# Optimization experiments

Hardware: AMD Instinct MI355X
Metric: run time of the kernel (lower is better)

Reference implementation:

```python
import jax, jax.numpy as jnp
import numpy as np

B, C, W, H = 4, 256, 64, 64
AC = C // 4  # attn channels


def setup_inputs() -> dict:
    key = jax.random.key(0)
    ks = jax.random.split(key, 4)
    x = jax.random.normal(ks[0], (B, C, W, H), dtype=jnp.float32)
    Wq = jax.random.normal(ks[1], (AC, C), dtype=jnp.float32) * (1.0 / np.sqrt(C))
    Wk = jax.random.normal(ks[2], (AC, C), dtype=jnp.float32) * (1.0 / np.sqrt(C))
    Wv = jax.random.normal(ks[3], (C, C), dtype=jnp.float32) * (1.0 / np.sqrt(C))
    bq = jnp.zeros((AC,), dtype=jnp.float32)
    bk = jnp.zeros((AC,), dtype=jnp.float32)
    bv = jnp.zeros((C,), dtype=jnp.float32)
    gamma = jnp.zeros((1,), dtype=jnp.float32)
    return {"x": x, "Wq": Wq, "bq": bq, "Wk": Wk, "bk": bk, "Wv": Wv, "bv": bv, "gamma": gamma}


def reference(x, Wq, bq, Wk, bk, Wv, bv, gamma):
    b, c, w, h = x.shape
    n = w * h
    xf = x.reshape(b, c, n)  # [B, C, N]
    # 1x1 convs == channel GEMMs
    q = jnp.einsum('oc,bcn->bon', Wq, xf) + bq[None, :, None]  # [B, AC, N]
    k = jnp.einsum('oc,bcn->bon', Wk, xf) + bk[None, :, None]  # [B, AC, N]
    v = jnp.einsum('oc,bcn->bon', Wv, xf) + bv[None, :, None]  # [B, C, N]
    # attn[b, i, j] = sum_c q[b, c, i] * k[b, c, j]  (query transposed)
    attn = jnp.einsum('bci,bcj->bij', q, k)  # [B, N, N]
    # NOTE: non-standard softmax over dim=1 (over query index i for each column j)
    attn = jax.nn.softmax(attn, axis=1)
    # attn_out = attn @ value.T  -> [B, N, C]
    attn_out = jnp.einsum('bij,bcj->bic', attn, v)
    attn_out = attn_out.reshape(b, w, h, c).transpose(0, 3, 1, 2)  # [B, C, W, H]
    return gamma[0] * attn_out + x
```

## Files before the change

### kernel.cpp

```cpp
#include <hip/hip_runtime.h>
#include <hip/hip_bf16.h>

#define BB 4
#define CC 256
#define NN 4096
#define AC2 64

typedef __attribute__((ext_vector_type(4))) float f32x4;
typedef __attribute__((ext_vector_type(8))) short bf16x8;

__device__ __forceinline__ short f2bf(float f) {
    unsigned u = __builtin_bit_cast(unsigned, f);
    u = u + 0x7FFFu + ((u >> 16) & 1u);
    return (short)(u >> 16);
}

__global__ __launch_bounds__(256) void qkv_kernel(
    const float* __restrict__ x,
    const float* __restrict__ Wq, const float* __restrict__ bq,
    const float* __restrict__ Wk, const float* __restrict__ bk,
    const float* __restrict__ Wv, const float* __restrict__ bv,
    short* __restrict__ Qt, short* __restrict__ Kt, short* __restrict__ V)
{
    __shared__ __align__(16) short Wl[384 * 72];
    __shared__ __align__(16) short Xl[64 * 72];
    const int bid = blockIdx.x;
    const int b = bid >> 6;
    const int n0 = (bid & 63) << 6;
    const int tid = threadIdx.x;
    const int lane = tid & 63, w = tid >> 6;

    f32x4 acc[6][4];
#pragma unroll
    for (int i = 0; i < 6; ++i)
#pragma unroll
        for (int j = 0; j < 4; ++j) acc[i][j] = (f32x4){0.f, 0.f, 0.f, 0.f};

    for (int ck = 0; ck < 4; ++ck) {
        const int c0 = ck * 64;
#pragma unroll 4
        for (int t = 0; t < 16; ++t) {
            int idx = tid + t * 256;
            int cr = idx >> 6, nc = idx & 63;
            float v = x[(((size_t)b * CC + c0 + cr) * NN) + n0 + nc];
            Xl[nc * 72 + cr] = f2bf(v);
        }
#pragma unroll 8
        for (int t = 0; t < 96; ++t) {
            int idx = tid + t * 256;
            int o = idx >> 6, cc2 = idx & 63;
            const float* row = (o < 64) ? (Wq + o * CC)
                             : (o < 128) ? (Wk + (o - 64) * CC)
                                         : (Wv + (o - 128) * CC);
            Wl[o * 72 + cc2] = f2bf(row[c0 + cc2]);
        }
        __syncthreads();
#pragma unroll
        for (int ks = 0; ks < 2; ++ks) {
            const int co = ks * 32 + ((lane >> 4) << 3);
            bf16x8 Bf[4];
#pragma unroll
            for (int nf = 0; nf < 4; ++nf)
                Bf[nf] = *(const bf16x8*)&Xl[(nf * 16 + (lane & 15)) * 72 + co];
#pragma unroll
            for (int of = 0; of < 6; ++of) {
                bf16x8 Af = *(const bf16x8*)&Wl[((w * 6 + of) * 16 + (lane & 15)) * 72 + co];
#pragma unroll
                for (int nf = 0; nf < 4; ++nf)
                    acc[of][nf] = __builtin_amdgcn_mfma_f32_16x16x32_bf16(
                        Af, Bf[nf], acc[of][nf], 0, 0, 0);
            }
        }
        __syncthreads();
    }
#pragma unroll
    for (int of = 0; of < 6; ++of) {
        const int obase = (w * 6 + of) * 16 + ((lane >> 4) << 2);
        float bias[4];
#pragma unroll
        for (int r = 0; r < 4; ++r) {
            int o = obase + r;
            bias[r] = (o < 64) ? bq[o] : (o < 128) ? bk[o - 64] : bv[o - 128];
        }
#pragma unroll
        for (int nf = 0; nf < 4; ++nf) {
            const int n = n0 + nf * 16 + (lane & 15);
            if (obase < 128) {
                short4 pk;
                pk.x = f2bf(acc[of][nf][0] + bias[0]);
                pk.y = f2bf(acc[of][nf][1] + bias[1]);
                pk.z = f2bf(acc[of][nf][2] + bias[2]);
                pk.w = f2bf(acc[of][nf][3] + bias[3]);
                short* dst = (obase < 64)
                    ? (Qt + ((size_t)b * NN + n) * AC2 + obase)
                    : (Kt + ((size_t)b * NN + n) * AC2 + (obase - 64));
                *(short4*)dst = pk;
            } else {
#pragma unroll
                for (int r = 0; r < 4; ++r) {
                    int o = obase + r - 128;
                    V[(((size_t)b * CC + o) * NN) + n] = f2bf(acc[of][nf][r] + bias[r]);
                }
            }
        }
    }
}

__global__ __launch_bounds__(256) void stats_kernel(
    const short* __restrict__ Qt, const short* __restrict__ Kt,
    float* __restrict__ mArr, float* __restrict__ rlArr)
{
    const int bid = blockIdx.x;
    const int b = bid >> 8;
    const int j0 = (bid & 255) << 4;
    const int tid = threadIdx.x;
    const int lane = tid & 63, w = tid >> 6;

    bf16x8 Bf[2];
#pragma unroll
    for (int ks = 0; ks < 2; ++ks)
        Bf[ks] = *(const bf16x8*)&Kt[((size_t)b * NN + j0 + (lane & 15)) * AC2 +
                                     ks * 32 + ((lane >> 4) << 3)];

    float m_run = -INFINITY, l_run = 0.f;
    for (int ii = 0; ii < 16; ++ii) {
        const int i0 = w * 1024 + ii * 64;
        f32x4 s[4];
#pragma unroll
        for (int f = 0; f < 4; ++f) {
            const size_t rowA = (size_t)b * NN + i0 + f * 16 + (lane & 15);
            bf16x8 A0 = *(const bf16x8*)&Qt[rowA * AC2 + ((lane >> 4) << 3)];
            bf16x8 A1 = *(const bf16x8*)&Qt[rowA * AC2 + 32 + ((lane >> 4) << 3)];
            f32x4 t = (f32x4){0.f, 0.f, 0.f, 0.f};
            t = __builtin_amdgcn_mfma_f32_16x16x32_bf16(A0, Bf[0], t, 0, 0, 0);
            t = __builtin_amdgcn_mfma_f32_16x16x32_bf16(A1, Bf[1], t, 0, 0, 0);
            s[f] = t;
        }
        float mx = s[0][0];
#pragma unroll
        for (int f = 0; f < 4; ++f)
#pragma unroll
            for (int r = 0; r < 4; ++r) mx = fmaxf(mx, s[f][r]);
        const float m_new = fmaxf(m_run, mx);
        float add = 0.f;
#pragma unroll
        for (int f = 0; f < 4; ++f)
#pragma unroll
            for (int r = 0; r < 4; ++r) add += __expf(s[f][r] - m_new);
        l_run = l_run * __expf(m_run - m_new) + add;
        m_run = m_new;
    }
#pragma unroll
    for (int off = 16; off <= 32; off <<= 1) {
        float m2 = __shfl_xor(m_run, off);
        float l2 = __shfl_xor(l_run, off);
        float mm = fmaxf(m_run, m2);
        l_run = l_run * __expf(m_run - mm) + l2 * __expf(m2 - mm);
        m_run = mm;
    }
    __shared__ float sm[4][16];
    __shared__ float sl[4][16];
    if (lane < 16) { sm[w][lane] = m_run; sl[w][lane] = l_run; }
    __syncthreads();
    if (tid < 16) {
        float m = sm[0][tid], l = sl[0][tid];
#pragma unroll
        for (int q = 1; q < 4; ++q) {
            float m2 = sm[q][tid], l2 = sl[q][tid];
            float mm = fmaxf(m, m2);
            l = l * __expf(m - mm) + l2 * __expf(m2 - mm);
            m = mm;
        }
        mArr[(size_t)b * NN + j0 + tid] = m;
        rlArr[(size_t)b * NN + j0 + tid] = 1.f / l;
    }
}

__global__ __launch_bounds__(256) void out_kernel(
    const short* __restrict__ Qt, const short* __restrict__ Kt,
    const short* __restrict__ V,
    const float* __restrict__ mArr, const float* __restrict__ rlArr,
    const float* __restrict__ x, const float* __restrict__ gamma,
    float* __restrict__ out)
{
    __shared__ __align__(16) short Pl[64 * 72];
    const int bid = blockIdx.x;
    const int b = bid >> 6;
    const int i0 = (bid & 63) << 6;
    const int tid = threadIdx.x;
    const int lane = tid & 63, w = tid >> 6;

    bf16x8 Aq[2];
#pragma unroll
    for (int ks = 0; ks < 2; ++ks)
        Aq[ks] = *(const bf16x8*)&Qt[((size_t)b * NN + i0 + w * 16 + (lane & 15)) * AC2 +
                                     ks * 32 + ((lane >> 4) << 3)];

    f32x4 acc[4][4];
#pragma unroll
    for (int i = 0; i < 4; ++i)
#pragma unroll
        for (int j = 0; j < 4; ++j) acc[i][j] = (f32x4){0.f, 0.f, 0.f, 0.f};

    for (int jt = 0; jt < 64; ++jt) {
        const int j0 = jt * 64;
#pragma unroll
        for (int jf = 0; jf < 4; ++jf) {
            const int j = j0 + jf * 16 + (lane & 15);
            f32x4 s = (f32x4){0.f, 0.f, 0.f, 0.f};
#pragma unroll
            for (int ks = 0; ks < 2; ++ks) {
                bf16x8 Bf = *(const bf16x8*)&Kt[((size_t)b * NN + j) * AC2 +
                                                ks * 32 + ((lane >> 4) << 3)];
                s = __builtin_amdgcn_mfma_f32_16x16x32_bf16(Aq[ks], Bf, s, 0, 0, 0);
            }
            const float mj = mArr[(size_t)b * NN + j];
            const float rj = rlArr[(size_t)b * NN + j];
#pragma unroll
            for (int r = 0; r < 4; ++r) {
                float p = __expf(s[r] - mj) * rj;
                Pl[(w * 16 + ((lane >> 4) << 2) + r) * 72 + jf * 16 + (lane & 15)] = f2bf(p);
            }
        }
        __syncthreads();
#pragma unroll
        for (int ks = 0; ks < 2; ++ks) {
            const int jj = j0 + ks * 32 + ((lane >> 4) << 3);
            bf16x8 Bv[4];
#pragma unroll
            for (int cf = 0; cf < 4; ++cf) {
                const int c = w * 64 + cf * 16 + (lane & 15);
                Bv[cf] = *(const bf16x8*)&V[(((size_t)b * CC + c) * NN) + jj];
            }
#pragma unroll
            for (int f = 0; f < 4; ++f) {
                bf16x8 Ap = *(const bf16x8*)&Pl[(f * 16 + (lane & 15)) * 72 +
                                                ks * 32 + ((lane >> 4) << 3)];
#pragma unroll
                for (int cf = 0; cf < 4; ++cf)
                    acc[f][cf] = __builtin_amdgcn_mfma_f32_16x16x32_bf16(
                        Ap, Bv[cf], acc[f][cf], 0, 0, 0);
            }
        }
        __syncthreads();
    }
    const float g = gamma[0];
#pragma unroll
    for (int f = 0; f < 4; ++f) {
#pragma unroll
        for (int cf = 0; cf < 4; ++cf) {
            const int c = w * 64 + cf * 16 + (lane & 15);
#pragma unroll
            for (int r = 0; r < 4; ++r) {
                const int i = i0 + f * 16 + ((lane >> 4) << 2) + r;
                const size_t idx = ((size_t)b * CC + c) * NN + i;
                out[idx] = g * acc[f][cf][r] + x[idx];
            }
        }
    }
}

extern "C" void kernel_launch(void* const* d_in, const int* in_sizes, int n_in,
                              void* d_out, int out_size, void* d_ws, size_t ws_size,
                              hipStream_t stream) {
    const float* x     = (const float*)d_in[0];
    const float* Wq    = (const float*)d_in[1];
    const float* bq    = (const float*)d_in[2];
    const float* Wk    = (const float*)d_in[3];
    const float* bk    = (const float*)d_in[4];
    const float* Wv    = (const float*)d_in[5];
    const float* bv    = (const float*)d_in[6];
    const float* gamma = (const float*)d_in[7];
    float* out = (float*)d_out;

    short* Qt = (short*)d_ws;
    short* Kt = Qt + (size_t)BB * NN * AC2;
    short* V  = Kt + (size_t)BB * NN * AC2;
    float* mArr  = (float*)(V + (size_t)BB * CC * NN);
    float* rlArr = mArr + (size_t)BB * NN;

    qkv_kernel<<<BB * 64, 256, 0, stream>>>(x, Wq, bq, Wk, bk, Wv, bv, Qt, Kt, V);
    stats_kernel<<<BB * 256, 256, 0, stream>>>(Qt, Kt, mArr, rlArr);
    out_kernel<<<BB * 64, 256, 0, stream>>>(Qt, Kt, V, mArr, rlArr, x, gamma, out);
}
```

Before: 359.6 us.

## Split attention output across channel slices and pre-convert weights to bf16

Adds a prep kernel that converts the weights to bf16 once, so the QKV kernel loads weight fragments directly instead of staging them in shared memory, and uses 512-thread blocks over 32-column tiles. The output kernel now splits channels into four slices per query tile, giving four times as many blocks. Each wave keeps its own P tile, which removes the block barriers, and output is written as coalesced float4 through a shared-memory transpose. Softmax stats are folded into a single log-sum-exp value, and block ids are XCD-swizzled. The cost is that QK^T and exp are recomputed four times, once per channel slice.

```diff
diff --git a/kernel.cpp b/kernel.cpp
--- a/kernel.cpp
+++ b/kernel.cpp
@@ -15,67 +15,79 @@
     return (short)(u >> 16);
 }
 
-__global__ __launch_bounds__(256) void qkv_kernel(
-    const float* __restrict__ x,
-    const float* __restrict__ Wq, const float* __restrict__ bq,
-    const float* __restrict__ Wk, const float* __restrict__ bk,
-    const float* __restrict__ Wv, const float* __restrict__ bv,
+__global__ __launch_bounds__(256) void prep_kernel(
+    const float* __restrict__ Wq, const float* __restrict__ Wk,
+    const float* __restrict__ Wv, short* __restrict__ Wb)
+{
+    const int idx = (blockIdx.x * 256 + threadIdx.x) * 4;
+    const int o = idx >> 8, c = idx & 255;
+    const float* row = (o < 64) ? (Wq + o * CC)
+                     : (o < 128) ? (Wk + (o - 64) * CC)
+                                 : (Wv + (o - 128) * CC);
+    float4 v = *(const float4*)&row[c];
+    short4 s4;
+    s4.x = f2bf(v.x); s4.y = f2bf(v.y); s4.z = f2bf(v.z); s4.w = f2bf(v.w);
+    *(short4*)&Wb[idx] = s4;
+}
+
+__global__ __launch_bounds__(512) void qkv_kernel(
+    const float* __restrict__ x, const short* __restrict__ Wb,
+    const float* __restrict__ bq, const float* __restrict__ bk,
+    const float* __restrict__ bv,
     short* __restrict__ Qt, short* __restrict__ Kt, short* __restrict__ V)
 {
-    __shared__ __align__(16) short Wl[384 * 72];
-    __shared__ __align__(16) short Xl[64 * 72];
-    const int bid = blockIdx.x;
-    const int b = bid >> 6;
-    const int n0 = (bid & 63) << 6;
+    __shared__ __align__(16) short Xl[32 * 72];
+    const int bid0 = blockIdx.x;
+    const int bid = ((bid0 & 7) << 6) | (bid0 >> 3);
+    const int b = bid >> 7;
+    const int n0 = (bid & 127) << 5;
     const int tid = threadIdx.x;
     const int lane = tid & 63, w = tid >> 6;
-
-    f32x4 acc[6][4];
-#pragma unroll
-    for (int i = 0; i < 6; ++i)
-#pragma unroll
-        for (int j = 0; j < 4; ++j) acc[i][j] = (f32x4){0.f, 0.f, 0.f, 0.f};
+    const int l15 = lane & 15, lh = lane >> 4;
+
+    f32x4 acc[3][2];
+#pragma unroll
+    for (int i = 0; i < 3; ++i)
+#pragma unroll
+        for (int j = 0; j < 2; ++j) acc[i][j] = (f32x4){0.f, 0.f, 0.f, 0.f};
 
     for (int ck = 0; ck < 4; ++ck) {
-        const int c0 = ck * 64;
-#pragma unroll 4
-        for (int t = 0; t < 16; ++t) {
-            int idx = tid + t * 256;
-            int cr = idx >> 6, nc = idx & 63;
-            float v = x[(((size_t)b * CC + c0 + cr) * NN) + n0 + nc];
-            Xl[nc * 72 + cr] = f2bf(v);
-        }
-#pragma unroll 8
-        for (int t = 0; t < 96; ++t) {
-            int idx = tid + t * 256;
-            int o = idx >> 6, cc2 = idx & 63;
-            const float* row = (o < 64) ? (Wq + o * CC)
-                             : (o < 128) ? (Wk + (o - 64) * CC)
-                                         : (Wv + (o - 128) * CC);
-            Wl[o * 72 + cc2] = f2bf(row[c0 + cc2]);
+        const int c0 = ck << 6;
+        bf16x8 Af[3][2];
+#pragma unroll
+        for (int of = 0; of < 3; ++of)
+#pragma unroll
+            for (int ks = 0; ks < 2; ++ks)
+                Af[of][ks] = *(const bf16x8*)&Wb[(size_t)(w * 48 + of * 16 + l15) * CC +
+                                                 c0 + ks * 32 + (lh << 3)];
+        {
+            const int cr = tid >> 3, q4 = tid & 7;
+            float4 v = *(const float4*)&x[((size_t)(b * CC + c0 + cr)) * NN + n0 + q4 * 4];
+            Xl[(q4 * 4 + 0) * 72 + cr] = f2bf(v.x);
+            Xl[(q4 * 4 + 1) * 72 + cr] = f2bf(v.y);
+            Xl[(q4 * 4 + 2) * 72 + cr] = f2bf(v.z);
+            Xl[(q4 * 4 + 3) * 72 + cr] = f2bf(v.w);
         }
         __syncthreads();
 #pragma unroll
         for (int ks = 0; ks < 2; ++ks) {
-            const int co = ks * 32 + ((lane >> 4) << 3);
-            bf16x8 Bf[4];
-#pragma unroll
-            for (int nf = 0; nf < 4; ++nf)
-                Bf[nf] = *(const bf16x8*)&Xl[(nf * 16 + (lane & 15)) * 72 + co];
-#pragma unroll
-            for (int of = 0; of < 6; ++of) {
-                bf16x8 Af = *(const bf16x8*)&Wl[((w * 6 + of) * 16 + (lane & 15)) * 72 + co];
-#pragma unroll
-                for (int nf = 0; nf < 4; ++nf)
+            const int co = ks * 32 + (lh << 3);
+            bf16x8 Bf[2];
+#pragma unroll
+            for (int nf = 0; nf < 2; ++nf)
+                Bf[nf] = *(const bf16x8*)&Xl[(nf * 16 + l15) * 72 + co];
+#pragma unroll
+            for (int of = 0; of < 3; ++of)
+#pragma unroll
+                for (int nf = 0; nf < 2; ++nf)
                     acc[of][nf] = __builtin_amdgcn_mfma_f32_16x16x32_bf16(
-                        Af, Bf[nf], acc[of][nf], 0, 0, 0);
-            }
+                        Af[of][ks], Bf[nf], acc[of][nf], 0, 0, 0);
         }
         __syncthreads();
     }
 #pragma unroll
-    for (int of = 0; of < 6; ++of) {
-        const int obase = (w * 6 + of) * 16 + ((lane >> 4) << 2);
+    for (int of = 0; of < 3; ++of) {
+        const int obase = w * 48 + of * 16 + (lh << 2);
         float bias[4];
 #pragma unroll
         for (int r = 0; r < 4; ++r) {
@@ -83,8 +95,8 @@
             bias[r] = (o < 64) ? bq[o] : (o < 128) ? bk[o - 64] : bv[o - 128];
         }
 #pragma unroll
-        for (int nf = 0; nf < 4; ++nf) {
-            const int n = n0 + nf * 16 + (lane & 15);
+        for (int nf = 0; nf < 2; ++nf) {
+            const int n = n0 + nf * 16 + l15;
             if (obase < 128) {
                 short4 pk;
                 pk.x = f2bf(acc[of][nf][0] + bias[0]);
@@ -108,9 +120,10 @@
 
 __global__ __launch_bounds__(256) void stats_kernel(
     const short* __restrict__ Qt, const short* __restrict__ Kt,
-    float* __restrict__ mArr, float* __restrict__ rlArr)
+    float* __restrict__ tArr)
 {
-    const int bid = blockIdx.x;
+    const int bid0 = blockIdx.x;
+    const int bid = ((bid0 & 7) << 7) | (bid0 >> 3);
     const int b = bid >> 8;
     const int j0 = (bid & 255) << 4;
     const int tid = threadIdx.x;
@@ -171,92 +184,94 @@
             l = l * __expf(m - mm) + l2 * __expf(m2 - mm);
             m = mm;
         }
-        mArr[(size_t)b * NN + j0 + tid] = m;
-        rlArr[(size_t)b * NN + j0 + tid] = 1.f / l;
+        tArr[(size_t)b * NN + j0 + tid] = m + __logf(l);
     }
 }
 
 __global__ __launch_bounds__(256) void out_kernel(
     const short* __restrict__ Qt, const short* __restrict__ Kt,
     const short* __restrict__ V,
-    const float* __restrict__ mArr, const float* __restrict__ rlArr,
+    const float* __restrict__ tArr,
     const float* __restrict__ x, const float* __restrict__ gamma,
     float* __restrict__ out)
 {
-    __shared__ __align__(16) short Pl[64 * 72];
-    const int bid = blockIdx.x;
-    const int b = bid >> 6;
-    const int i0 = (bid & 63) << 6;
+    __shared__ __align__(16) short Pl[4 * 16 * 72];
+    __shared__ __align__(16) float Pf[4 * 16 * 69];
+    const int bid0 = blockIdx.x;
+    const int bid = ((bid0 & 7) << 7) | (bid0 >> 3);
+    const int cs = bid & 3;
+    const int itile = (bid >> 2) & 63;
+    const int b = bid >> 8;
+    const int i0 = itile << 6, c0 = cs << 6;
     const int tid = threadIdx.x;
     const int lane = tid & 63, w = tid >> 6;
+    const int l15 = lane & 15, lh = lane >> 4;
+    const int iw = i0 + (w << 4);
+    short* Plw = Pl + w * (16 * 72);
+
+    const short* Ktb = Kt + (size_t)b * NN * AC2;
+    const float* tb = tArr + (size_t)b * NN;
+    const short* Vb = V + ((size_t)b * CC + c0) * NN;
 
     bf16x8 Aq[2];
 #pragma unroll
     for (int ks = 0; ks < 2; ++ks)
-        Aq[ks] = *(const bf16x8*)&Qt[((size_t)b * NN + i0 + w * 16 + (lane & 15)) * AC2 +
-                                     ks * 32 + ((lane >> 4) << 3)];
-
-    f32x4 acc[4][4];
-#pragma unroll
-    for (int i = 0; i < 4; ++i)
-#pragma unroll
-        for (int j = 0; j < 4; ++j) acc[i][j] = (f32x4){0.f, 0.f, 0.f, 0.f};
+        Aq[ks] = *(const bf16x8*)&Qt[((size_t)b * NN + iw + l15) * AC2 +
+                                     ks * 32 + (lh << 3)];
+
+    f32x4 acc[4];
+#pragma unroll
+    for (int i = 0; i < 4; ++i) acc[i] = (f32x4){0.f, 0.f, 0.f, 0.f};
 
     for (int jt = 0; jt < 64; ++jt) {
         const int j0 = jt * 64;
 #pragma unroll
         for (int jf = 0; jf < 4; ++jf) {
-            const int j = j0 + jf * 16 + (lane & 15);
+            const int j = j0 + jf * 16 + l15;
             f32x4 s = (f32x4){0.f, 0.f, 0.f, 0.f};
 #pragma unroll
             for (int ks = 0; ks < 2; ++ks) {
-                bf16x8 Bf = *(const bf16x8*)&Kt[((size_t)b * NN + j) * AC2 +
-                                                ks * 32 + ((lane >> 4) << 3)];
+                bf16x8 Bf = *(const bf16x8*)&Ktb[(size_t)j * AC2 + ks * 32 + (lh << 3)];
                 s = __builtin_amdgcn_mfma_f32_16x16x32_bf16(Aq[ks], Bf, s, 0, 0, 0);
             }
-            const float mj = mArr[(size_t)b * NN + j];
-            const float rj = rlArr[(size_t)b * NN + j];
-#pragma unroll
-            for (int r = 0; r < 4; ++r) {
-                float p = __expf(s[r] - mj) * rj;
-                Pl[(w * 16 + ((lane >> 4) << 2) + r) * 72 + jf * 16 + (lane & 15)] = f2bf(p);
+            const float tj = tb[j];
+#pragma unroll
+            for (int r = 0; r < 4; ++r)
+                Plw[(lh * 4 + r) * 72 + jf * 16 + l15] = f2bf(__expf(s[r] - tj));
+        }
+#pragma unroll
+        for (int ks = 0; ks < 2; ++ks) {
+            const int jj = j0 + ks * 32 + (lh << 3);
+            bf16x8 Ap = *(const bf16x8*)&Plw[l15 * 72 + ks * 32 + (lh << 3)];
+#pragma unroll
+            for (int cf = 0; cf < 4; ++cf) {
+                bf16x8 Bv = *(const bf16x8*)&Vb[(size_t)(cf * 16 + l15) * NN + jj];
+                acc[cf] = __builtin_amdgcn_mfma_f32_16x16x32_bf16(Ap, Bv, acc[cf], 0, 0, 0);
             }
         }
-        __syncthreads();
-#pragma unroll
-        for (int ks = 0; ks < 2; ++ks) {
-            const int jj = j0 + ks * 32 + ((lane >> 4) << 3);
-            bf16x8 Bv[4];
-#pragma unroll
-            for (int cf = 0; cf < 4; ++cf) {
-                const int c = w * 64 + cf * 16 + (lane & 15);
-                Bv[cf] = *(const bf16x8*)&V[(((size_t)b * CC + c) * NN) + jj];
-            }
-#pragma unroll
-            for (int f = 0; f < 4; ++f) {
-                bf16x8 Ap = *(const bf16x8*)&Pl[(f * 16 + (lane & 15)) * 72 +
-                                                ks * 32 + ((lane >> 4) << 3)];
-#pragma unroll
-                for (int cf = 0; cf < 4; ++cf)
-                    acc[f][cf] = __builtin_amdgcn_mfma_f32_16x16x32_bf16(
-                        Ap, Bv[cf], acc[f][cf], 0, 0, 0);
-            }
-        }
-        __syncthreads();
-    }
+    }
+    float* Pfw = Pf + w * (16 * 69);
+#pragma unroll
+    for (int cf = 0; cf < 4; ++cf)
+#pragma unroll
+        for (int r = 0; r < 4; ++r)
+            Pfw[(lh * 4 + r) * 69 + cf * 16 + l15] = acc[cf][r];
     const float g = gamma[0];
-#pragma unroll
-    for (int f = 0; f < 4; ++f) {
-#pragma unroll
-        for (int cf = 0; cf < 4; ++cf) {
-            const int c = w * 64 + cf * 16 + (lane & 15);
-#pragma unroll
-            for (int r = 0; r < 4; ++r) {
-                const int i = i0 + f * 16 + ((lane >> 4) << 2) + r;
-                const size_t idx = ((size_t)b * CC + c) * NN + i;
-                out[idx] = g * acc[f][cf][r] + x[idx];
-            }
-        }
+    const size_t obase = ((size_t)(b * CC + c0 + lane)) * NN + iw;
+#pragma unroll
+    for (int e4 = 0; e4 < 4; ++e4) {
+        float4 v;
+        v.x = Pfw[(e4 * 4 + 0) * 69 + lane];
+        v.y = Pfw[(e4 * 4 + 1) * 69 + lane];
+        v.z = Pfw[(e4 * 4 + 2) * 69 + lane];
+        v.w = Pfw[(e4 * 4 + 3) * 69 + lane];
+        float4 xv = *(const float4*)&x[obase + e4 * 4];
+        float4 o;
+        o.x = g * v.x + xv.x;
+        o.y = g * v.y + xv.y;
+        o.z = g * v.z + xv.z;
+        o.w = g * v.w + xv.w;
+        *(float4*)&out[obase + e4 * 4] = o;
     }
 }
 
@@ -276,10 +291,11 @@
     short* Qt = (short*)d_ws;
     short* Kt = Qt + (size_t)BB * NN * AC2;
     short* V  = Kt + (size_t)BB * NN * AC2;
-    float* mArr  = (float*)(V + (size_t)BB * CC * NN);
-    float* rlArr = mArr + (size_t)BB * NN;
-
-    qkv_kernel<<<BB * 64, 256, 0, stream>>>(x, Wq, bq, Wk, bk, Wv, bv, Qt, Kt, V);
-    stats_kernel<<<BB * 256, 256, 0, stream>>>(Qt, Kt, mArr, rlArr);
-    out_kernel<<<BB * 64, 256, 0, stream>>>(Qt, Kt, V, mArr, rlArr, x, gamma, out);
-}
+    float* tArr = (float*)(V + (size_t)BB * CC * NN);
+    short* Wb = (short*)(tArr + (size_t)BB * NN);
+
+    prep_kernel<<<96, 256, 0, stream>>>(Wq, Wk, Wv, Wb);
+    qkv_kernel<<<BB * 128, 512, 0, stream>>>(x, Wb, bq, bk, bv, Qt, Kt, V);
+    stats_kernel<<<BB * 256, 256, 0, stream>>>(Qt, Kt, tArr);
+    out_kernel<<<BB * 256, 256, 0, stream>>>(Qt, Kt, V, tArr, x, gamma, out);
+}
```

Measured after the change: 612.2 us. +70.3%, slower.
